# Kernel optimization log

Hardware: AMD Instinct MI355X
Metric: run time of the kernel (lower is better)

## Reference

```python
import jax, jax.numpy as jnp
import numpy as np

N, D = 8192, 256
EPS = 1e-12  # guards sqrt(0) on the diagonal


def setup_inputs() -> dict:
    key = jax.random.key(0)
    kx, = jax.random.split(key, 1)
    x = jax.random.normal(kx, (N, D), dtype=jnp.float32)
    threshold = jnp.zeros((1,), dtype=jnp.float32)  # nn.Parameter(torch.zeros(1))
    t = jnp.ones((1,), dtype=jnp.float32)           # nn.Parameter(torch.ones(1))
    return {"x": x, "threshold": threshold, "t": t}


def reference(x, threshold, t):
    # Sigmoid-like branch: pairwise euclidean distance without materializing [N,N,D].
    # |x_i - x_j|^2 summed over D == ||x_i||^2 + ||x_j||^2 - 2 x_i.x_j  (abs is a no-op under squaring)
    sq = jnp.sum(x * x, axis=1)  # [N]
    dist2 = sq[:, None] + sq[None, :] - 2.0 * (x @ x.T)  # [N, N]
    dist = jnp.sqrt(jnp.maximum(dist2, EPS))
    diff = (dist + threshold) * t  # broadcast scalar params
    return 1.0 - jax.nn.sigmoid(diff)
```

## Files before the change

kernel.cpp:

```cpp
#include <hip/hip_runtime.h>
#include <cstdint>
#include <cstddef>

#define NN 8192
#define DD 256

typedef __bf16 bf16x8 __attribute__((ext_vector_type(8)));
typedef float f32x4 __attribute__((ext_vector_type(4)));

__global__ __launch_bounds__(256) void prep_kernel(const float* __restrict__ x,
                                                   unsigned short* __restrict__ xb,
                                                   float* __restrict__ sq) {
    const int row = blockIdx.x;
    const int c = threadIdx.x;
    const size_t idx = (size_t)row * DD + c;
    const float v = x[idx];
    unsigned int u = __float_as_uint(v);
    unsigned int r = (u + 0x7FFFu + ((u >> 16) & 1u)) >> 16;
    xb[idx] = (unsigned short)r;

    float p = v * v;
#pragma unroll
    for (int off = 32; off > 0; off >>= 1) p += __shfl_down(p, off, 64);
    __shared__ float wsum[4];
    const int wave = c >> 6, lane = c & 63;
    if (lane == 0) wsum[wave] = p;
    __syncthreads();
    if (c == 0) sq[row] = wsum[0] + wsum[1] + wsum[2] + wsum[3];
}

__global__ __launch_bounds__(256) void gemm_sig_kernel(
    const unsigned short* __restrict__ Xb, const float* __restrict__ sq,
    const float* __restrict__ thrp, const float* __restrict__ tp,
    float* __restrict__ out) {
    __shared__ __align__(16) unsigned short lA[128 * 32];
    __shared__ __align__(16) unsigned short lB[128 * 32];

    const int tid = threadIdx.x;
    const int wave = tid >> 6;
    const int lane = tid & 63;

    const int brow = blockIdx.y;
    const int bcol = blockIdx.x;
    const int wrow = (wave >> 1) * 64;
    const int wcol = (wave & 1) * 64;

    const int srow = lane >> 2;
    const int scol = (lane & 3) * 8;

    const size_t rowA0 = (size_t)brow * 128;
    const size_t rowB0 = (size_t)bcol * 128;

    const unsigned short* gA0 = Xb + (rowA0 + wave * 32 + srow) * DD + scol;
    const unsigned short* gA1 = gA0 + 16 * DD;
    const unsigned short* gB0 = Xb + (rowB0 + wave * 32 + srow) * DD + scol;
    const unsigned short* gB1 = gB0 + 16 * DD;
    unsigned short* ldsA0 = &lA[(wave * 2 + 0) * 512];
    unsigned short* ldsA1 = &lA[(wave * 2 + 1) * 512];
    unsigned short* ldsB0 = &lB[(wave * 2 + 0) * 512];
    unsigned short* ldsB1 = &lB[(wave * 2 + 1) * 512];

    f32x4 acc[4][4] = {};

    const int fr = lane & 15;
    const int fk = (lane >> 4) * 8;

#define KSTEP(KK)                                                                  \
    do {                                                                           \
        __syncthreads();                                                           \
        __builtin_amdgcn_global_load_lds(                                          \
            (const __attribute__((address_space(1))) void*)gA0,                    \
            (__attribute__((address_space(3))) void*)ldsA0, 16, (KK) * 64, 0);     \
        __builtin_amdgcn_global_load_lds(                                          \
            (const __attribute__((address_space(1))) void*)gA1,                    \
            (__attribute__((address_space(3))) void*)ldsA1, 16, (KK) * 64, 0);     \
        __builtin_amdgcn_global_load_lds(                                          \
            (const __attribute__((address_space(1))) void*)gB0,                    \
            (__attribute__((address_space(3))) void*)ldsB0, 16, (KK) * 64, 0);     \
        __builtin_amdgcn_global_load_lds(                                          \
            (const __attribute__((address_space(1))) void*)gB1,                    \
            (__attribute__((address_space(3))) void*)ldsB1, 16, (KK) * 64, 0);     \
        __syncthreads();                                                           \
        bf16x8 af[4], bfv[4];                                                      \
        _Pragma("unroll") for (int t = 0; t < 4; ++t) {                            \
            af[t] = *(const bf16x8*)&lA[(wrow + t * 16 + fr) * 32 + fk];           \
            bfv[t] = *(const bf16x8*)&lB[(wcol + t * 16 + fr) * 32 + fk];          \
        }                                                                          \
        _Pragma("unroll") for (int ti = 0; ti < 4; ++ti)                           \
            _Pragma("unroll") for (int tj = 0; tj < 4; ++tj)                       \
                acc[ti][tj] = __builtin_amdgcn_mfma_f32_16x16x32_bf16(             \
                    af[ti], bfv[tj], acc[ti][tj], 0, 0, 0);                        \
    } while (0)

    KSTEP(0); KSTEP(1); KSTEP(2); KSTEP(3);
    KSTEP(4); KSTEP(5); KSTEP(6); KSTEP(7);
#undef KSTEP

    const float tv = tp[0];
    const float thr_t = thrp[0] * tv;
    const int c0 = lane & 15;
    const int r0q = (lane >> 4) * 4;

    float sqi[16], sqj[4];
#pragma unroll
    for (int ti = 0; ti < 4; ++ti)
#pragma unroll
        for (int rg = 0; rg < 4; ++rg)
            sqi[ti * 4 + rg] = sq[rowA0 + wrow + ti * 16 + r0q + rg];
#pragma unroll
    for (int tj = 0; tj < 4; ++tj) sqj[tj] = sq[rowB0 + wcol + tj * 16 + c0];

    float* ob = out + (rowA0 + wrow + r0q) * NN + (rowB0 + wcol + c0);

    if (brow != bcol) {
#pragma unroll
        for (int ti = 0; ti < 4; ++ti)
#pragma unroll
            for (int tj = 0; tj < 4; ++tj)
#pragma unroll
                for (int rg = 0; rg < 4; ++rg) {
                    float d2 = fmaf(-2.0f, acc[ti][tj][rg], sqi[ti * 4 + rg] + sqj[tj]);
                    d2 = fmaxf(d2, 1e-12f);
                    const float dist = __builtin_amdgcn_sqrtf(d2);
                    const float e = __expf(fmaf(dist, tv, thr_t));
                    ob[(size_t)(ti * 16 + rg) * NN + tj * 16] =
                        __builtin_amdgcn_rcpf(1.0f + e);
                }
    } else {
#pragma unroll
        for (int ti = 0; ti < 4; ++ti)
#pragma unroll
            for (int tj = 0; tj < 4; ++tj)
#pragma unroll
                for (int rg = 0; rg < 4; ++rg) {
                    const int rloc = wrow + ti * 16 + r0q + rg;
                    const int cloc = wcol + tj * 16 + c0;
                    float d2 = fmaf(-2.0f, acc[ti][tj][rg], sqi[ti * 4 + rg] + sqj[tj]);
                    if (rloc == cloc) d2 = 0.0f;
                    d2 = fmaxf(d2, 1e-12f);
                    const float dist = __builtin_amdgcn_sqrtf(d2);
                    const float e = __expf(fmaf(dist, tv, thr_t));
                    ob[(size_t)(ti * 16 + rg) * NN + tj * 16] =
                        __builtin_amdgcn_rcpf(1.0f + e);
                }
    }
}

extern "C" void kernel_launch(void* const* d_in, const int* in_sizes, int n_in,
                              void* d_out, int out_size, void* d_ws, size_t ws_size,
                              hipStream_t stream) {
    const float* x = (const float*)d_in[0];
    const float* threshold = (const float*)d_in[1];
    const float* t = (const float*)d_in[2];
    float* out = (float*)d_out;

    unsigned short* xb = (unsigned short*)d_ws;
    float* sq = (float*)((char*)d_ws + (size_t)NN * DD * sizeof(unsigned short));

    prep_kernel<<<NN, 256, 0, stream>>>(x, xb, sq);
    dim3 grid(NN / 128, NN / 128);
    gemm_sig_kernel<<<grid, 256, 0, stream>>>(xb, sq, threshold, t, out);
}
```

Before: 299.4 us.

## Store bf16 X in k-octet-major layout and load MFMA fragments directly from global

The prep kernel now writes the bf16 copy of X in a layout where each 8-element k-chunk is contiguous per row (octet-major), processing 8 rows per block with vectorized float4 loads and a 32-lane reduction. The GEMM kernel drops LDS staging and both barriers per k-step. It loads MFMA operand fragments directly from global memory into registers, double-buffered across k-steps. This removes LDS traffic and synchronisation, at the cost of every wave re-reading its A and B fragments from L2/global with no intra-block sharing, and higher register pressure.

```diff
diff --git a/kernel.cpp b/kernel.cpp
--- a/kernel.cpp
+++ b/kernel.cpp
@@ -7,35 +7,37 @@
 
 typedef __bf16 bf16x8 __attribute__((ext_vector_type(8)));
 typedef float f32x4 __attribute__((ext_vector_type(4)));
+typedef unsigned short ushort8 __attribute__((ext_vector_type(8)));
 
 __global__ __launch_bounds__(256) void prep_kernel(const float* __restrict__ x,
-                                                   unsigned short* __restrict__ xb,
+                                                   unsigned short* __restrict__ xbt,
                                                    float* __restrict__ sq) {
-    const int row = blockIdx.x;
-    const int c = threadIdx.x;
-    const size_t idx = (size_t)row * DD + c;
-    const float v = x[idx];
-    unsigned int u = __float_as_uint(v);
-    unsigned int r = (u + 0x7FFFu + ((u >> 16) & 1u)) >> 16;
-    xb[idx] = (unsigned short)r;
-
-    float p = v * v;
+    const int t = threadIdx.x;
+    const int oct = t & 31;
+    const int rl = t >> 5;
+    const int row = blockIdx.x * 8 + rl;
+    const float4* xp = (const float4*)(x + (size_t)row * DD + oct * 8);
+    const float4 a = xp[0], b = xp[1];
+    const float vs[8] = {a.x, a.y, a.z, a.w, b.x, b.y, b.z, b.w};
+    ushort8 o;
+    float p = 0.0f;
 #pragma unroll
-    for (int off = 32; off > 0; off >>= 1) p += __shfl_down(p, off, 64);
-    __shared__ float wsum[4];
-    const int wave = c >> 6, lane = c & 63;
-    if (lane == 0) wsum[wave] = p;
-    __syncthreads();
-    if (c == 0) sq[row] = wsum[0] + wsum[1] + wsum[2] + wsum[3];
+    for (int i = 0; i < 8; ++i) {
+        const float v = vs[i];
+        const unsigned int u = __float_as_uint(v);
+        o[i] = (unsigned short)((u + 0x7FFFu + ((u >> 16) & 1u)) >> 16);
+        p = fmaf(v, v, p);
+    }
+    *(ushort8*)(xbt + ((size_t)oct * NN + row) * 8) = o;
+#pragma unroll
+    for (int off = 16; off > 0; off >>= 1) p += __shfl_down(p, off, 32);
+    if (oct == 0) sq[row] = p;
 }
 
 __global__ __launch_bounds__(256) void gemm_sig_kernel(
-    const unsigned short* __restrict__ Xb, const float* __restrict__ sq,
+    const unsigned short* __restrict__ XbT, const float* __restrict__ sq,
     const float* __restrict__ thrp, const float* __restrict__ tp,
     float* __restrict__ out) {
-    __shared__ __align__(16) unsigned short lA[128 * 32];
-    __shared__ __align__(16) unsigned short lB[128 * 32];
-
     const int tid = threadIdx.x;
     const int wave = tid >> 6;
     const int lane = tid & 63;
@@ -45,56 +47,43 @@
     const int wrow = (wave >> 1) * 64;
     const int wcol = (wave & 1) * 64;
 
-    const int srow = lane >> 2;
-    const int scol = (lane & 3) * 8;
+    const int fr = lane & 15;
+    const int q = lane >> 4;
 
     const size_t rowA0 = (size_t)brow * 128;
     const size_t rowB0 = (size_t)bcol * 128;
 
-    const unsigned short* gA0 = Xb + (rowA0 + wave * 32 + srow) * DD + scol;
-    const unsigned short* gA1 = gA0 + 16 * DD;
-    const unsigned short* gB0 = Xb + (rowB0 + wave * 32 + srow) * DD + scol;
-    const unsigned short* gB1 = gB0 + 16 * DD;
-    unsigned short* ldsA0 = &lA[(wave * 2 + 0) * 512];
-    unsigned short* ldsA1 = &lA[(wave * 2 + 1) * 512];
-    unsigned short* ldsB0 = &lB[(wave * 2 + 0) * 512];
-    unsigned short* ldsB1 = &lB[(wave * 2 + 1) * 512];
+    const unsigned short* pA = XbT + ((size_t)q * NN + rowA0 + wrow + fr) * 8;
+    const unsigned short* pB = XbT + ((size_t)q * NN + rowB0 + wcol + fr) * 8;
+    const size_t kkStride = (size_t)4 * NN * 8;
 
     f32x4 acc[4][4] = {};
+    bf16x8 afp[2][4], bfp[2][4];
 
-    const int fr = lane & 15;
-    const int fk = (lane >> 4) * 8;
-
-#define KSTEP(KK)                                                                  \
-    do {                                                                           \
-        __syncthreads();                                                           \
-        __builtin_amdgcn_global_load_lds(                                          \
-            (const __attribute__((address_space(1))) void*)gA0,                    \
-            (__attribute__((address_space(3))) void*)ldsA0, 16, (KK) * 64, 0);     \
-        __builtin_amdgcn_global_load_lds(                                          \
-            (const __attribute__((address_space(1))) void*)gA1,                    \
-            (__attribute__((address_space(3))) void*)ldsA1, 16, (KK) * 64, 0);     \
-        __builtin_amdgcn_global_load_lds(                                          \
-            (const __attribute__((address_space(1))) void*)gB0,                    \
-            (__attribute__((address_space(3))) void*)ldsB0, 16, (KK) * 64, 0);     \
-        __builtin_amdgcn_global_load_lds(                                          \
-            (const __attribute__((address_space(1))) void*)gB1,                    \
-            (__attribute__((address_space(3))) void*)ldsB1, 16, (KK) * 64, 0);     \
-        __syncthreads();                                                           \
-        bf16x8 af[4], bfv[4];                                                      \
-        _Pragma("unroll") for (int t = 0; t < 4; ++t) {                            \
-            af[t] = *(const bf16x8*)&lA[(wrow + t * 16 + fr) * 32 + fk];           \
-            bfv[t] = *(const bf16x8*)&lB[(wcol + t * 16 + fr) * 32 + fk];          \
-        }                                                                          \
-        _Pragma("unroll") for (int ti = 0; ti < 4; ++ti)                           \
-            _Pragma("unroll") for (int tj = 0; tj < 4; ++tj)                       \
-                acc[ti][tj] = __builtin_amdgcn_mfma_f32_16x16x32_bf16(             \
-                    af[ti], bfv[tj], acc[ti][tj], 0, 0, 0);                        \
-    } while (0)
-
-    KSTEP(0); KSTEP(1); KSTEP(2); KSTEP(3);
-    KSTEP(4); KSTEP(5); KSTEP(6); KSTEP(7);
-#undef KSTEP
+#pragma unroll
+    for (int t = 0; t < 4; ++t) {
+        afp[0][t] = *(const bf16x8*)(pA + t * 128);
+        bfp[0][t] = *(const bf16x8*)(pB + t * 128);
+    }
+#pragma unroll
+    for (int kk = 0; kk < 8; ++kk) {
+        const int cur = kk & 1, nxt = cur ^ 1;
+        if (kk < 7) {
+            const unsigned short* nA = pA + (size_t)(kk + 1) * kkStride;
+            const unsigned short* nB = pB + (size_t)(kk + 1) * kkStride;
+#pragma unroll
+            for (int t = 0; t < 4; ++t) {
+                afp[nxt][t] = *(const bf16x8*)(nA + t * 128);
+                bfp[nxt][t] = *(const bf16x8*)(nB + t * 128);
+            }
+        }
+#pragma unroll
+        for (int ti = 0; ti < 4; ++ti)
+#pragma unroll
+            for (int tj = 0; tj < 4; ++tj)
+                acc[ti][tj] = __builtin_amdgcn_mfma_f32_16x16x32_bf16(
+                    afp[cur][ti], bfp[cur][tj], acc[ti][tj], 0, 0, 0);
+    }
 
     const float tv = tp[0];
     const float thr_t = thrp[0] * tv;
@@ -154,10 +143,10 @@
     const float* t = (const float*)d_in[2];
     float* out = (float*)d_out;
 
-    unsigned short* xb = (unsigned short*)d_ws;
+    unsigned short* xbt = (unsigned short*)d_ws;
     float* sq = (float*)((char*)d_ws + (size_t)NN * DD * sizeof(unsigned short));
 
-    prep_kernel<<<NN, 256, 0, stream>>>(x, xb, sq);
+    prep_kernel<<<NN / 8, 256, 0, stream>>>(x, xbt, sq);
     dim3 grid(NN / 128, NN / 128);
-    gemm_sig_kernel<<<grid, 256, 0, stream>>>(xb, sq, threshold, t, out);
+    gemm_sig_kernel<<<grid, 256, 0, stream>>>(xbt, sq, threshold, t, out);
 }
```

After: 299.2 us. Within noise of the previous version (-0.1%).
